# Kernel tuning notes

Hardware: AMD Instinct MI355X
Metric: run time of the kernel (lower is better)

The kernel has to match this reference:

```python
import jax, jax.numpy as jnp
import numpy as np

B, F, T, Z, Y, X = 1, 8, 5, 16, 96, 96
N_RAYS = 32768   # n_rays_scan
K = 128          # n_points_ray
NEAR_PLANE = 0.01
C = F * Z        # conv channels after folding Z into channel dim


def setup_inputs() -> dict:
    key = jax.random.key(0)
    ks = jax.random.split(key, 6)
    vol = jax.random.normal(ks[0], (B, F, T, Z, Y, X), jnp.float32)
    # ray origins inside the normalized unit-cube scene
    rays_o = jax.random.uniform(ks[1], (T, N_RAYS, 3), jnp.float32, 0.1, 0.9)
    rd = jax.random.normal(ks[2], (T, N_RAYS, 3), jnp.float32)
    rays_d = rd / jnp.linalg.norm(rd, axis=-1, keepdims=True)
    conv_w = jax.random.normal(ks[3], (C, C, 3, 3, 3), jnp.float32) * (1.0 / np.sqrt(C * 27))
    conv_b = jnp.zeros((C,), jnp.float32)
    dens_w = jax.random.normal(ks[4], (F, 1), jnp.float32) * (1.0 / np.sqrt(F))
    dens_b = jnp.zeros((1,), jnp.float32)
    return dict(curr_feat_volume=vol, ray_start=rays_o, ray_direction=rays_d,
                conv_w=conv_w, conv_b=conv_b, dens_w=dens_w, dens_b=dens_b)


def _trilinear(vol, pts):
    """vol: [F,Z,Y,X]; pts: [...,3] with (x,y,z) in [0,1]. Returns [..., F]."""
    Fc, Zs, Ys, Xs = vol.shape
    gx = jnp.clip(pts[..., 0], 0.0, 1.0) * (Xs - 1)
    gy = jnp.clip(pts[..., 1], 0.0, 1.0) * (Ys - 1)
    gz = jnp.clip(pts[..., 2], 0.0, 1.0) * (Zs - 1)
    x0 = jnp.floor(gx).astype(jnp.int32); x1 = jnp.minimum(x0 + 1, Xs - 1)
    y0 = jnp.floor(gy).astype(jnp.int32); y1 = jnp.minimum(y0 + 1, Ys - 1)
    z0 = jnp.floor(gz).astype(jnp.int32); z1 = jnp.minimum(z0 + 1, Zs - 1)
    fx = gx - x0; fy = gy - y0; fz = gz - z0
    out = 0.0
    for zi, wz in ((z0, 1 - fz), (z1, fz)):
        for yi, wy in ((y0, 1 - fy), (y1, fy)):
            for xi, wx in ((x0, 1 - fx), (x1, fx)):
                out = out + vol[:, zi, yi, xi] * (wz * wy * wx)[None]
    return jnp.moveaxis(out, 0, -1)


def _render_t(vol_t, o, d, dens_w, dens_b):
    """One timestep: vol_t [F,Z,Y,X], o/d [N,3] -> depth [N,1]."""
    # SceneCollider: AABB [0,1]^3 with near_plane clamp
    t1 = (0.0 - o) / d
    t2 = (1.0 - o) / d
    near = jnp.max(jnp.minimum(t1, t2), axis=-1, keepdims=True)
    far = jnp.min(jnp.maximum(t1, t2), axis=-1, keepdims=True)
    near = jnp.maximum(near, NEAR_PLANE)
    far = jnp.maximum(far, near + 1e-6)
    # UniformSampler (deterministic bins)
    bins = jnp.linspace(0.0, 1.0, K + 1, dtype=jnp.float32)
    ts = near + bins[None, :] * (far - near)          # [N,K+1]
    starts = ts[:, :-1, None]                          # [N,K,1]
    ends = ts[:, 1:, None]
    mids = 0.5 * (starts + ends)
    pts = o[:, None, :] + d[:, None, :] * mids         # [N,K,3]
    # DensityField: trilinear feature gather + linear + softplus
    feats = _trilinear(vol_t, pts)                     # [N,K,F]
    density = jax.nn.softplus(feats @ dens_w + dens_b) # [N,K,1]
    # weights / transmittance (alpha compositing)
    deltas = ends - starts
    dd = density * deltas
    trans = jnp.exp(-jnp.concatenate([jnp.zeros_like(dd[:, :1]),
                                      jnp.cumsum(dd[:, :-1], axis=1)], axis=1))
    alpha = 1.0 - jnp.exp(-dd)
    weights = alpha * trans                            # [N,K,1]
    # DepthRenderer
    eps = 1e-10
    depth = jnp.sum(weights * starts, axis=-2) / (jnp.sum(weights, axis=-2) + eps)
    depth = jnp.clip(depth, starts.min(), starts.max())
    return depth                                       # [N,1]


def reference(curr_feat_volume, ray_start, ray_direction, conv_w, conv_b, dens_w, dens_b):
    # fold Z into channels and run dense Conv3d over (T,Y,X)
    x = jnp.transpose(curr_feat_volume, (0, 1, 3, 2, 4, 5)).reshape(B, F * Z, T, Y, X)
    y = jax.lax.conv_general_dilated(
        x, conv_w, window_strides=(1, 1, 1), padding='SAME',
        dimension_numbers=('NCDHW', 'OIDHW', 'NCDHW'))
    y = y + conv_b[None, :, None, None, None]
    future = jnp.transpose(y.reshape(B, F, Z, T, Y, X), (0, 3, 1, 2, 4, 5))  # [B,T,F,Z,Y,X]
    vols = future[0]                                   # [T,F,Z,Y,X]
    depth = jax.vmap(lambda v, o, d: _render_t(v, o, d, dens_w, dens_b))(
        vols, ray_start, ray_direction)                # [T,N,1]
    return depth
```

## Files before the change

### kernel.cpp

```cpp
#include <hip/hip_runtime.h>
#include <hip/hip_fp16.h>
#include <cstdint>
#include <cstddef>

#define T_DIM 5
#define F_DIM 8
#define Z_DIM 16
#define Y_DIM 96
#define X_DIM 96
#define NRAYS 32768
#define K_SAMP 128


struct __align__(16) Cell { __half2 h0, h1, h2, h3; };

typedef __attribute__((ext_vector_type(4))) float     f32x4;
typedef __attribute__((ext_vector_type(8))) _Float16  f16x8;

__device__ __forceinline__ float fexp2(float x) { return __builtin_amdgcn_exp2f(x); }
__device__ __forceinline__ float flog2(float x) { return __builtin_amdgcn_logf(x); }

__global__ __launch_bounds__(256) void setup_kernel(
        const float* __restrict__ xin, __half* __restrict__ inp,
        const float* __restrict__ w, const float* __restrict__ cb,
        const float* __restrict__ dw, __half* __restrict__ wB, float* __restrict__ bR,
        const float* __restrict__ ro, const float* __restrict__ rd,
        float* __restrict__ nearA, float* __restrict__ farA) {
    int b = blockIdx.x;
    if (b < 480) {
        __shared__ __half lds[96 * 136];
        int t = b / 96, y = b - (b / 96) * 96;
        for (int i = threadIdx.x; i < 12288; i += 256) {
            int row = i / 96;
            int x   = i - row * 96;
            int f = row >> 4, z = row & 15;
            float v = xin[(((size_t)(f * 5 + t) * 16 + z) * 96 + y) * 96 + x];
            lds[x * 136 + row] = __float2half(v);
        }
        __syncthreads();
        __half* ob = inp + ((size_t)(t * 96 + y) * 96) * 128;
        for (int c = threadIdx.x; c < 1536; c += 256) {
            int x = c >> 4, sub = c & 15;
            uint4 v = *(const uint4*)(lds + x * 136 + sub * 8);
            *(uint4*)(ob + (size_t)x * 128 + sub * 8) = v;
        }
    } else if (b < 696) {
        int i = (b - 480) * 256 + threadIdx.x;
        if (i < 16) {
            float s = 0.f;
            #pragma unroll
            for (int f = 0; f < 8; ++f) s += cb[f * 16 + i] * dw[f];
            bR[i] = s;
        }
        int cs  = i & 31;
        int zo  = (i >> 5) & 15;
        int pt  = i >> 9;
        int p   = pt / 27;
        int tap = pt - p * 27;
        int ci  = p * 32 + cs;
        float s = 0.f;
        #pragma unroll
        for (int f = 0; f < 8; ++f)
            s += w[(size_t)((f * 16 + zo) * 128 + ci) * 27 + tap] * dw[f];
        wB[i] = __float2half(s);
    } else {
        int gid = (b - 696) * 256 + threadIdx.x;
        const float* o = ro + (size_t)gid * 3;
        const float* d = rd + (size_t)gid * 3;
        float ox = o[0], oy = o[1], oz = o[2];
        float dx = d[0], dy = d[1], dz = d[2];
        float t1x = (0.f - ox) / dx, t2x = (1.f - ox) / dx;
        float t1y = (0.f - oy) / dy, t2y = (1.f - oy) / dy;
        float t1z = (0.f - oz) / dz, t2z = (1.f - oz) / dz;
        float nr = fmaxf(fmaxf(fminf(t1x, t2x), fminf(t1y, t2y)), fminf(t1z, t2z));
        float fr = fminf(fminf(fmaxf(t1x, t2x), fmaxf(t1y, t2y)), fmaxf(t1z, t2z));
        nr = fmaxf(nr, 0.01f);
        fr = fmaxf(fr, nr + 1e-6f);
        nearA[gid] = nr;
        farA[gid]  = fr;
    }
}

__global__ __launch_bounds__(128) void conv_mfma_kernel(
        const __half* __restrict__ inp, const __half* __restrict__ wB,
        const float* __restrict__ bR, float* __restrict__ fld) {
    int bid = blockIdx.x;
    int wg  = (bid & 7) * 90 + (bid >> 3);
    int xs  = wg % 3;
    int rem = wg / 3;
    int yp  = rem % 48;
    int t   = rem / 48;
    int xseg = xs * 32, y0 = yp * 2;

    __shared__ __half lds[2][12 * 34 * 32];
    const int w    = threadIdx.x >> 6;
    const int lane = threadIdx.x & 63;
    const int l15  = lane & 15;
    const int ksub = lane >> 4;

    const int xl0 = threadIdx.x >> 2, sub0 = threadIdx.x & 3;
    const int xg0 = xseg + xl0 - 1;
    const bool xok0 = (unsigned)xg0 < 96u;
    const int glo0 = xg0 * 128 + sub0 * 8;
    const int lof0 = xl0 * 32 + ((sub0 ^ ((xl0 >> 1) & 3)) << 3);
    const int q    = threadIdx.x / 12;
    const int rowh = threadIdx.x - q * 12;
    const int xl1  = 32 + (q >> 2), sub1 = q & 3;
    const int xg1  = xseg + xl1 - 1;
    const bool hwr = (q < 8);
    const bool hld = hwr && ((unsigned)xg1 < 96u);
    const int glo1 = xg1 * 128 + sub1 * 8;
    const int lof1 = xl1 * 32 + ((sub1 ^ ((xl1 >> 1) & 3)) << 3);

    int offA[3];
    #pragma unroll
    for (int kx = 0; kx < 3; ++kx) {
        int X = l15 + kx;
        offA[kx] = X * 32 + ((ksub ^ ((X >> 1) & 3)) << 3);
    }

    uint4 vm[12];
    uint4 vh;
    f32x4 acc0 = {0.f, 0.f, 0.f, 0.f};
    f32x4 acc1 = {0.f, 0.f, 0.f, 0.f};

    #pragma unroll
    for (int r = 0; r < 12; ++r) {
        int tt = t + (r >> 2) - 1;
        int yy = y0 + (r & 3) - 1;
        bool rok = ((unsigned)tt < 5u) & ((unsigned)yy < 96u);
        int rbase = (tt * 96 + yy) * 12288;
        uint4 v = {0u, 0u, 0u, 0u};
        if (rok & xok0) v = *(const uint4*)(inp + rbase + glo0);
        vm[r] = v;
    }
    {
        int tt = t + (rowh >> 2) - 1;
        int yy = y0 + (rowh & 3) - 1;
        bool rok = ((unsigned)tt < 5u) & ((unsigned)yy < 96u);
        int rbase = (tt * 96 + yy) * 12288;
        uint4 v = {0u, 0u, 0u, 0u};
        if (rok & hld) v = *(const uint4*)(inp + rbase + glo1);
        vh = v;
    }

    #pragma unroll
    for (int p = 0; p < 4; ++p) {
        __half* L = &lds[p & 1][0];
        #pragma unroll
        for (int r = 0; r < 12; ++r)
            *(uint4*)(L + r * 1088 + lof0) = vm[r];
        if (hwr)
            *(uint4*)(L + rowh * 1088 + lof1) = vh;
        __syncthreads();

        if (p < 3) {
            #pragma unroll
            for (int r = 0; r < 12; ++r) {
                int tt = t + (r >> 2) - 1;
                int yy = y0 + (r & 3) - 1;
                bool rok = ((unsigned)tt < 5u) & ((unsigned)yy < 96u);
                int rbase = (tt * 96 + yy) * 12288 + ((p + 1) << 5);
                uint4 v = {0u, 0u, 0u, 0u};
                if (rok & xok0) v = *(const uint4*)(inp + rbase + glo0);
                vm[r] = v;
            }
            {
                int tt = t + (rowh >> 2) - 1;
                int yy = y0 + (rowh & 3) - 1;
                bool rok = ((unsigned)tt < 5u) & ((unsigned)yy < 96u);
                int rbase = (tt * 96 + yy) * 12288 + ((p + 1) << 5);
                uint4 v = {0u, 0u, 0u, 0u};
                if (rok & hld) v = *(const uint4*)(inp + rbase + glo1);
                vh = v;
            }
        }

        const __half* wp_base = wB + (size_t)p * 13824 + l15 * 32 + ksub * 8;
        #pragma unroll
        for (int kt = 0; kt < 3; ++kt) {
            #pragma unroll
            for (int ky = 0; ky < 3; ++ky) {
                const __half* lrow = L + (kt * 4 + w + ky) * 1088;
                #pragma unroll
                for (int kx = 0; kx < 3; ++kx) {
                    int tap = (kt * 3 + ky) * 3 + kx;
                    f16x8 aw = *(const f16x8*)(wp_base + tap * 512);
                    f16x8 b0 = *(const f16x8*)(lrow + offA[kx]);
                    acc0 = __builtin_amdgcn_mfma_f32_16x16x32_f16(aw, b0, acc0, 0, 0, 0);
                    f16x8 b1 = *(const f16x8*)(lrow + offA[kx] + 512);
                    acc1 = __builtin_amdgcn_mfma_f32_16x16x32_f16(aw, b1, acc1, 0, 0, 0);
                }
            }
        }
    }

    int yw = y0 + w;
    #pragma unroll
    for (int r = 0; r < 4; ++r) {
        int zo = ksub * 4 + r;
        float bz = bR[zo];
        size_t o = (((size_t)t * 16 + zo) * 96 + yw) * 96 + xseg + l15;
        fld[o]      = acc0[r] + bz;
        fld[o + 16] = acc1[r] + bz;
    }
}

__global__ __launch_bounds__(256) void pack_kernel(
        const float* __restrict__ fld, Cell* __restrict__ cellp) {
    int i = blockIdx.x * 256 + threadIdx.x;
    if (i >= 737280) return;
    int x = i % 96;
    int r = i / 96;
    int y = r % 96;
    int r2 = r / 96;
    int z = r2 % 16;
    int t = r2 / 16;
    const float* ft = fld + (size_t)t * 147456;
    int xp = min(x + 1, 95);
    int yr0 = y * 96, yr1 = min(y + 1, 95) * 96;
    int zr0 = z * 9216, zr1 = min(z + 1, 15) * 9216;
    float c000 = ft[zr0 + yr0 + x], c001 = ft[zr0 + yr0 + xp];
    float c010 = ft[zr0 + yr1 + x], c011 = ft[zr0 + yr1 + xp];
    float c100 = ft[zr1 + yr0 + x], c101 = ft[zr1 + yr0 + xp];
    float c110 = ft[zr1 + yr1 + x], c111 = ft[zr1 + yr1 + xp];
    Cell cl;
    cl.h0 = __floats2half2_rn(c000, c001 - c000);
    cl.h1 = __floats2half2_rn(c010, c011 - c010);
    cl.h2 = __floats2half2_rn(c100, c101 - c100);
    cl.h3 = __floats2half2_rn(c110, c111 - c110);
    cellp[i] = cl;
}

__global__ __launch_bounds__(256) void render_kernel(
        const float* __restrict__ ro, const float* __restrict__ rd,
        const Cell* __restrict__ cellp,
        const float* __restrict__ nearA, const float* __restrict__ farA,
        const float* __restrict__ dens_b, float* __restrict__ out) {
    int b = blockIdx.x;
    int b7 = b & 7, bhi = b >> 3;
    int t, seg;
    if (b7 < 5) { t = b7; seg = bhi; }
    else { int j = (b7 - 5) * 640 + bhi; t = j / 384; seg = 640 + j % 384; }
    int c = threadIdx.x & 7;
    int ray = t * NRAYS + seg * 32 + (threadIdx.x >> 3);

    const float* o = ro + (size_t)ray * 3;
    const float* d = rd + (size_t)ray * 3;
    float ox = o[0], oy = o[1], oz = o[2];
    float dx = d[0], dy = d[1], dz = d[2];
    float nr = nearA[ray], fr = farA[ray];
    const Cell* vt = cellp + (size_t)t * 147456;
    const float L2E = 1.4426950408889634f;
    float db2 = dens_b[0] * L2E;

    float span = fr - nr;
    float step = span * 0.0078125f;
    float s  = fmaf((float)(c * 16), step, nr);
    float mid = s + 0.5f * step;
    float pxg = fmaf(dx, mid, ox) * 95.f;
    float pyg = fmaf(dy, mid, oy) * 95.f;
    float pzg = fmaf(dz, mid, oz) * 15.f;
    float ddxg = dx * step * 95.f, ddyg = dy * step * 95.f, ddzg = dz * step * 15.f;

    float num = 0.f, den = 0.f, A2 = 0.f;
    float trans = 1.f;
    int pidx = -1;
    Cell cl;
    for (int kk = 0; kk < 16; ++kk) {
        int x0 = min(max((int)pxg, 0), 94);
        int y0 = min(max((int)pyg, 0), 94);
        int z0 = min(max((int)pzg, 0), 14);
        float fx = pxg - (float)x0, fy = pyg - (float)y0, fz = pzg - (float)z0;

        int idx = z0 * 9216 + y0 * 96 + x0;
        if (idx != pidx) {
            pidx = idx;
            cl = vt[idx];
        }

        float v00 = fmaf(fx, __half2float(__high2half(cl.h0)), __half2float(__low2half(cl.h0)));
        float v01 = fmaf(fx, __half2float(__high2half(cl.h1)), __half2float(__low2half(cl.h1)));
        float v10 = fmaf(fx, __half2float(__high2half(cl.h2)), __half2float(__low2half(cl.h2)));
        float v11 = fmaf(fx, __half2float(__high2half(cl.h3)), __half2float(__low2half(cl.h3)));
        float v0  = fmaf(fy, v01 - v00, v00);
        float v1  = fmaf(fy, v11 - v10, v10);
        float pre2 = fmaf(fmaf(fz, v1 - v0, v0), L2E, db2);

        float u = fexp2(-fabsf(pre2));
        float dens2 = fmaxf(pre2, 0.f) + flog2(1.f + u);
        float dd2 = dens2 * step;
        float ex = fexp2(-dd2);
        float wgt = (1.f - ex) * trans;
        num = fmaf(wgt, s, num);
        den += wgt;
        trans *= ex;
        A2 += dd2;
        s += step; pxg += ddxg; pyg += ddyg; pzg += ddzg;
    }
    int lane = threadIdx.x & 63;
    int qb = lane & ~7;
    float P = 0.f;
    #pragma unroll
    for (int j = 0; j < 7; ++j) {
        float Aj = __shfl(A2, qb + j, 64);
        P += (c > j) ? Aj : 0.f;
    }
    float sc = fexp2(-P);
    float numc = num * sc;
    float denc = den * sc;
    numc += __shfl_xor(numc, 1, 64);
    numc += __shfl_xor(numc, 2, 64);
    numc += __shfl_xor(numc, 4, 64);
    denc += __shfl_xor(denc, 1, 64);
    denc += __shfl_xor(denc, 2, 64);
    denc += __shfl_xor(denc, 4, 64);
    if (c == 0) {
        float depth = numc / (denc + 1e-10f);
        float slast = fmaf(0.9921875f, span, nr);
        depth = fminf(fmaxf(depth, nr), slast);
        out[ray] = depth;
    }
}

extern "C" void kernel_launch(void* const* d_in, const int* in_sizes, int n_in,
                              void* d_out, int out_size, void* d_ws, size_t ws_size,
                              hipStream_t stream) {
    const float* vol = (const float*)d_in[0];
    const float* ro  = (const float*)d_in[1];
    const float* rd  = (const float*)d_in[2];
    const float* cw  = (const float*)d_in[3];
    const float* cb  = (const float*)d_in[4];
    const float* dw  = (const float*)d_in[5];
    const float* dbp = (const float*)d_in[6];
    float* out = (float*)d_out;

    float* ws      = (float*)d_ws;
    float* fld     = ws;
    __half* inp    = (__half*)(ws + 737280);
    Cell*  cellp   = (Cell*)(ws + 737280);
    __half* wB     = (__half*)(ws + 737280 + 2949120);
    float* bR      = ws + 737280 + 2949120 + 27648;
    float* nearA   = bR + 32;
    float* farA    = nearA + 163840;

    hipLaunchKernelGGL(setup_kernel, dim3(1336), dim3(256), 0, stream,
                       vol, inp, cw, cb, dw, wB, bR, ro, rd, nearA, farA);
    hipLaunchKernelGGL(conv_mfma_kernel, dim3(720), dim3(128), 0, stream,
                       inp, wB, bR, fld);
    hipLaunchKernelGGL(pack_kernel, dim3(2880), dim3(256), 0, stream, fld, cellp);
    hipLaunchKernelGGL(render_kernel, dim3(5120), dim3(256), 0, stream,
                       ro, rd, cellp, nearA, farA, dbp, out);
}
```

Measured before the change: 161.4 us.

## Drop LDS staging in conv; read input directly from global with finer tiles

```diff
diff --git a/kernel.cpp b/kernel.cpp
--- a/kernel.cpp
+++ b/kernel.cpp
@@ -81,128 +81,77 @@
     }
 }
 
-__global__ __launch_bounds__(128) void conv_mfma_kernel(
+__global__ __launch_bounds__(128, 4) void conv_mfma_kernel(
         const __half* __restrict__ inp, const __half* __restrict__ wB,
         const float* __restrict__ bR, float* __restrict__ fld) {
     int bid = blockIdx.x;
-    int wg  = (bid & 7) * 90 + (bid >> 3);
+    int wg  = (bid & 7) * 180 + (bid >> 3);
     int xs  = wg % 3;
     int rem = wg / 3;
-    int yp  = rem % 48;
-    int t   = rem / 48;
-    int xseg = xs * 32, y0 = yp * 2;
-
-    __shared__ __half lds[2][12 * 34 * 32];
-    const int w    = threadIdx.x >> 6;
+    int y   = rem % 96;
+    int t   = rem / 96;
+
+    const int xt   = threadIdx.x >> 6;
     const int lane = threadIdx.x & 63;
     const int l15  = lane & 15;
     const int ksub = lane >> 4;
-
-    const int xl0 = threadIdx.x >> 2, sub0 = threadIdx.x & 3;
-    const int xg0 = xseg + xl0 - 1;
-    const bool xok0 = (unsigned)xg0 < 96u;
-    const int glo0 = xg0 * 128 + sub0 * 8;
-    const int lof0 = xl0 * 32 + ((sub0 ^ ((xl0 >> 1) & 3)) << 3);
-    const int q    = threadIdx.x / 12;
-    const int rowh = threadIdx.x - q * 12;
-    const int xl1  = 32 + (q >> 2), sub1 = q & 3;
-    const int xg1  = xseg + xl1 - 1;
-    const bool hwr = (q < 8);
-    const bool hld = hwr && ((unsigned)xg1 < 96u);
-    const int glo1 = xg1 * 128 + sub1 * 8;
-    const int lof1 = xl1 * 32 + ((sub1 ^ ((xl1 >> 1) & 3)) << 3);
-
-    int offA[3];
-    #pragma unroll
-    for (int kx = 0; kx < 3; ++kx) {
-        int X = l15 + kx;
-        offA[kx] = X * 32 + ((ksub ^ ((X >> 1) & 3)) << 3);
-    }
-
-    uint4 vm[12];
-    uint4 vh;
-    f32x4 acc0 = {0.f, 0.f, 0.f, 0.f};
-    f32x4 acc1 = {0.f, 0.f, 0.f, 0.f};
-
-    #pragma unroll
-    for (int r = 0; r < 12; ++r) {
-        int tt = t + (r >> 2) - 1;
-        int yy = y0 + (r & 3) - 1;
-        bool rok = ((unsigned)tt < 5u) & ((unsigned)yy < 96u);
-        int rbase = (tt * 96 + yy) * 12288;
-        uint4 v = {0u, 0u, 0u, 0u};
-        if (rok & xok0) v = *(const uint4*)(inp + rbase + glo0);
-        vm[r] = v;
-    }
-    {
-        int tt = t + (rowh >> 2) - 1;
-        int yy = y0 + (rowh & 3) - 1;
-        bool rok = ((unsigned)tt < 5u) & ((unsigned)yy < 96u);
-        int rbase = (tt * 96 + yy) * 12288;
-        uint4 v = {0u, 0u, 0u, 0u};
-        if (rok & hld) v = *(const uint4*)(inp + rbase + glo1);
-        vh = v;
-    }
+    const int xb   = xs * 32 + xt * 16;
+
+    const bool ok0 = (xb + l15 - 1) >= 0;
+    const bool ok2 = (xb + l15 + 1) < 96;
+    const int xh0 = max(xb + l15 - 1, 0) << 7;
+    const int xh1 = (xb + l15) << 7;
+    const int xh2 = min(xb + l15 + 1, 95) << 7;
+
+    f32x4 accA = {0.f, 0.f, 0.f, 0.f};
+    f32x4 accB = {0.f, 0.f, 0.f, 0.f};
+    const int ko = ksub * 8;
 
     #pragma unroll
     for (int p = 0; p < 4; ++p) {
-        __half* L = &lds[p & 1][0];
-        #pragma unroll
-        for (int r = 0; r < 12; ++r)
-            *(uint4*)(L + r * 1088 + lof0) = vm[r];
-        if (hwr)
-            *(uint4*)(L + rowh * 1088 + lof1) = vh;
-        __syncthreads();
-
-        if (p < 3) {
-            #pragma unroll
-            for (int r = 0; r < 12; ++r) {
-                int tt = t + (r >> 2) - 1;
-                int yy = y0 + (r & 3) - 1;
-                bool rok = ((unsigned)tt < 5u) & ((unsigned)yy < 96u);
-                int rbase = (tt * 96 + yy) * 12288 + ((p + 1) << 5);
-                uint4 v = {0u, 0u, 0u, 0u};
-                if (rok & xok0) v = *(const uint4*)(inp + rbase + glo0);
-                vm[r] = v;
-            }
-            {
-                int tt = t + (rowh >> 2) - 1;
-                int yy = y0 + (rowh & 3) - 1;
-                bool rok = ((unsigned)tt < 5u) & ((unsigned)yy < 96u);
-                int rbase = (tt * 96 + yy) * 12288 + ((p + 1) << 5);
-                uint4 v = {0u, 0u, 0u, 0u};
-                if (rok & hld) v = *(const uint4*)(inp + rbase + glo1);
-                vh = v;
-            }
-        }
-
-        const __half* wp_base = wB + (size_t)p * 13824 + l15 * 32 + ksub * 8;
+        const __half* wpb = wB + p * 13824 + l15 * 32 + ko;
         #pragma unroll
         for (int kt = 0; kt < 3; ++kt) {
+            int tt = t + kt - 1;
+            if ((unsigned)tt >= 5u) continue;
             #pragma unroll
             for (int ky = 0; ky < 3; ++ky) {
-                const __half* lrow = L + (kt * 4 + w + ky) * 1088;
-                #pragma unroll
-                for (int kx = 0; kx < 3; ++kx) {
-                    int tap = (kt * 3 + ky) * 3 + kx;
-                    f16x8 aw = *(const f16x8*)(wp_base + tap * 512);
-                    f16x8 b0 = *(const f16x8*)(lrow + offA[kx]);
-                    acc0 = __builtin_amdgcn_mfma_f32_16x16x32_f16(aw, b0, acc0, 0, 0, 0);
-                    f16x8 b1 = *(const f16x8*)(lrow + offA[kx] + 512);
-                    acc1 = __builtin_amdgcn_mfma_f32_16x16x32_f16(aw, b1, acc1, 0, 0, 0);
+                int yy = y + ky - 1;
+                if ((unsigned)yy >= 96u) continue;
+                const __half* rb = inp + (size_t)(tt * 96 + yy) * 12288 + (p << 5) + ko;
+                const int tapb = (kt * 3 + ky) * 3;
+                {
+                    f16x8 aw = *(const f16x8*)(wpb + tapb * 512);
+                    uint4 bv = *(const uint4*)(rb + xh0);
+                    if (!ok0) bv = make_uint4(0u, 0u, 0u, 0u);
+                    f16x8 bb = *(f16x8*)&bv;
+                    if (tapb & 1) accB = __builtin_amdgcn_mfma_f32_16x16x32_f16(aw, bb, accB, 0, 0, 0);
+                    else          accA = __builtin_amdgcn_mfma_f32_16x16x32_f16(aw, bb, accA, 0, 0, 0);
+                }
+                {
+                    f16x8 aw = *(const f16x8*)(wpb + (tapb + 1) * 512);
+                    f16x8 bb = *(const f16x8*)(rb + xh1);
+                    if ((tapb + 1) & 1) accB = __builtin_amdgcn_mfma_f32_16x16x32_f16(aw, bb, accB, 0, 0, 0);
+                    else                accA = __builtin_amdgcn_mfma_f32_16x16x32_f16(aw, bb, accA, 0, 0, 0);
+                }
+                {
+                    f16x8 aw = *(const f16x8*)(wpb + (tapb + 2) * 512);
+                    uint4 bv = *(const uint4*)(rb + xh2);
+                    if (!ok2) bv = make_uint4(0u, 0u, 0u, 0u);
+                    f16x8 bb = *(f16x8*)&bv;
+                    if ((tapb + 2) & 1) accB = __builtin_amdgcn_mfma_f32_16x16x32_f16(aw, bb, accB, 0, 0, 0);
+                    else                accA = __builtin_amdgcn_mfma_f32_16x16x32_f16(aw, bb, accA, 0, 0, 0);
                 }
             }
         }
     }
 
-    int yw = y0 + w;
     #pragma unroll
     for (int r = 0; r < 4; ++r) {
         int zo = ksub * 4 + r;
         float bz = bR[zo];
-        size_t o = (((size_t)t * 16 + zo) * 96 + yw) * 96 + xseg + l15;
-        fld[o]      = acc0[r] + bz;
-        fld[o + 16] = acc1[r] + bz;
+        size_t o = (((size_t)t * 16 + zo) * 96 + y) * 96 + xb + l15;
+        fld[o] = accA[r] + accB[r] + bz;
     }
 }
 
@@ -346,7 +295,7 @@
 
     hipLaunchKernelGGL(setup_kernel, dim3(1336), dim3(256), 0, stream,
                        vol, inp, cw, cb, dw, wB, bR, ro, rd, nearA, farA);
-    hipLaunchKernelGGL(conv_mfma_kernel, dim3(720), dim3(128), 0, stream,
+    hipLaunchKernelGGL(conv_mfma_kernel, dim3(1440), dim3(128), 0, stream,
                        inp, wB, bR, fld);
     hipLaunchKernelGGL(pack_kernel, dim3(2880), dim3(256), 0, stream, fld, cellp);
     hipLaunchKernelGGL(render_kernel, dim3(5120), dim3(256), 0, stream,
```

Result: slower. 195.5 us (+21.1%).

## Split conv reduction over input-channel chunks across blocks and add combine kernel

Applied to the files above, without the earlier changes.

```diff
diff --git a/kernel.cpp b/kernel.cpp
--- a/kernel.cpp
+++ b/kernel.cpp
@@ -83,16 +83,18 @@
 
 __global__ __launch_bounds__(128) void conv_mfma_kernel(
         const __half* __restrict__ inp, const __half* __restrict__ wB,
-        const float* __restrict__ bR, float* __restrict__ fld) {
+        float* __restrict__ part) {
     int bid = blockIdx.x;
-    int wg  = (bid & 7) * 90 + (bid >> 3);
-    int xs  = wg % 3;
-    int rem = wg / 3;
+    int wg  = (bid & 7) * 360 + (bid >> 3);
+    int p   = wg & 3;
+    int wq  = wg >> 2;
+    int xs  = wq % 3;
+    int rem = wq / 3;
     int yp  = rem % 48;
     int t   = rem / 48;
     int xseg = xs * 32, y0 = yp * 2;
 
-    __shared__ __half lds[2][12 * 34 * 32];
+    __shared__ __half lds[12 * 34 * 32];
     const int w    = threadIdx.x >> 6;
     const int lane = threadIdx.x & 63;
     const int l15  = lane & 15;
@@ -101,7 +103,7 @@
     const int xl0 = threadIdx.x >> 2, sub0 = threadIdx.x & 3;
     const int xg0 = xseg + xl0 - 1;
     const bool xok0 = (unsigned)xg0 < 96u;
-    const int glo0 = xg0 * 128 + sub0 * 8;
+    const int glo0 = xg0 * 128 + sub0 * 8 + (p << 5);
     const int lof0 = xl0 * 32 + ((sub0 ^ ((xl0 >> 1) & 3)) << 3);
     const int q    = threadIdx.x / 12;
     const int rowh = threadIdx.x - q * 12;
@@ -109,7 +111,7 @@
     const int xg1  = xseg + xl1 - 1;
     const bool hwr = (q < 8);
     const bool hld = hwr && ((unsigned)xg1 < 96u);
-    const int glo1 = xg1 * 128 + sub1 * 8;
+    const int glo1 = xg1 * 128 + sub1 * 8 + (p << 5);
     const int lof1 = xl1 * 32 + ((sub1 ^ ((xl1 >> 1) & 3)) << 3);
 
     int offA[3];
@@ -120,10 +122,6 @@
     }
 
     uint4 vm[12];
-    uint4 vh;
-    f32x4 acc0 = {0.f, 0.f, 0.f, 0.f};
-    f32x4 acc1 = {0.f, 0.f, 0.f, 0.f};
-
     #pragma unroll
     for (int r = 0; r < 12; ++r) {
         int tt = t + (r >> 2) - 1;
@@ -134,76 +132,67 @@
         if (rok & xok0) v = *(const uint4*)(inp + rbase + glo0);
         vm[r] = v;
     }
+    uint4 vh = {0u, 0u, 0u, 0u};
     {
         int tt = t + (rowh >> 2) - 1;
         int yy = y0 + (rowh & 3) - 1;
         bool rok = ((unsigned)tt < 5u) & ((unsigned)yy < 96u);
         int rbase = (tt * 96 + yy) * 12288;
-        uint4 v = {0u, 0u, 0u, 0u};
-        if (rok & hld) v = *(const uint4*)(inp + rbase + glo1);
-        vh = v;
-    }
-
-    #pragma unroll
-    for (int p = 0; p < 4; ++p) {
-        __half* L = &lds[p & 1][0];
+        if (rok & hld) vh = *(const uint4*)(inp + rbase + glo1);
+    }
+    #pragma unroll
+    for (int r = 0; r < 12; ++r)
+        *(uint4*)(lds + r * 1088 + lof0) = vm[r];
+    if (hwr)
+        *(uint4*)(lds + rowh * 1088 + lof1) = vh;
+    __syncthreads();
+
+    f32x4 acc0 = {0.f, 0.f, 0.f, 0.f};
+    f32x4 acc1 = {0.f, 0.f, 0.f, 0.f};
+    const __half* wp_base = wB + (size_t)p * 13824 + l15 * 32 + ksub * 8;
+    #pragma unroll
+    for (int kt = 0; kt < 3; ++kt) {
         #pragma unroll
-        for (int r = 0; r < 12; ++r)
-            *(uint4*)(L + r * 1088 + lof0) = vm[r];
-        if (hwr)
-            *(uint4*)(L + rowh * 1088 + lof1) = vh;
-        __syncthreads();
-
-        if (p < 3) {
+        for (int ky = 0; ky < 3; ++ky) {
+            const __half* lrow = lds + (kt * 4 + w + ky) * 1088;
             #pragma unroll
-            for (int r = 0; r < 12; ++r) {
-                int tt = t + (r >> 2) - 1;
-                int yy = y0 + (r & 3) - 1;
-                bool rok = ((unsigned)tt < 5u) & ((unsigned)yy < 96u);
-                int rbase = (tt * 96 + yy) * 12288 + ((p + 1) << 5);
-                uint4 v = {0u, 0u, 0u, 0u};
-                if (rok & xok0) v = *(const uint4*)(inp + rbase + glo0);
-                vm[r] = v;
+            for (int kx = 0; kx < 3; ++kx) {
+                int tap = (kt * 3 + ky) * 3 + kx;
+                f16x8 aw = *(const f16x8*)(wp_base + tap * 512);
+                f16x8 b0 = *(const f16x8*)(lrow + offA[kx]);
+                acc0 = __builtin_amdgcn_mfma_f32_16x16x32_f16(aw, b0, acc0, 0, 0, 0);
+                f16x8 b1 = *(const f16x8*)(lrow + offA[kx] + 512);
+                acc1 = __builtin_amdgcn_mfma_f32_16x16x32_f16(aw, b1, acc1, 0, 0, 0);
             }
-            {
-                int tt = t + (rowh >> 2) - 1;
-                int yy = y0 + (rowh & 3) - 1;
-                bool rok = ((unsigned)tt < 5u) & ((unsigned)yy < 96u);
-                int rbase = (tt * 96 + yy) * 12288 + ((p + 1) << 5);
-                uint4 v = {0u, 0u, 0u, 0u};
-                if (rok & hld) v = *(const uint4*)(inp + rbase + glo1);
-                vh = v;
-            }
-        }
-
-        const __half* wp_base = wB + (size_t)p * 13824 + l15 * 32 + ksub * 8;
-        #pragma unroll
-        for (int kt = 0; kt < 3; ++kt) {
-            #pragma unroll
-            for (int ky = 0; ky < 3; ++ky) {
-                const __half* lrow = L + (kt * 4 + w + ky) * 1088;
-                #pragma unroll
-                for (int kx = 0; kx < 3; ++kx) {
-                    int tap = (kt * 3 + ky) * 3 + kx;
-                    f16x8 aw = *(const f16x8*)(wp_base + tap * 512);
-                    f16x8 b0 = *(const f16x8*)(lrow + offA[kx]);
-                    acc0 = __builtin_amdgcn_mfma_f32_16x16x32_f16(aw, b0, acc0, 0, 0, 0);
-                    f16x8 b1 = *(const f16x8*)(lrow + offA[kx] + 512);
-                    acc1 = __builtin_amdgcn_mfma_f32_16x16x32_f16(aw, b1, acc1, 0, 0, 0);
-                }
-            }
         }
     }
 
     int yw = y0 + w;
+    float* po = part + (size_t)p * 737280;
     #pragma unroll
     for (int r = 0; r < 4; ++r) {
         int zo = ksub * 4 + r;
-        float bz = bR[zo];
         size_t o = (((size_t)t * 16 + zo) * 96 + yw) * 96 + xseg + l15;
-        fld[o]      = acc0[r] + bz;
-        fld[o + 16] = acc1[r] + bz;
-    }
+        po[o]      = acc0[r];
+        po[o + 16] = acc1[r];
+    }
+}
+
+__global__ __launch_bounds__(256) void combine_kernel(
+        const float* __restrict__ part, const float* __restrict__ bR,
+        float* __restrict__ fld) {
+    int i = blockIdx.x * 256 + threadIdx.x;
+    if (i >= 184320) return;
+    int z = (i / 2304) & 15;
+    float b = bR[z];
+    float4 r = make_float4(b, b, b, b);
+    const float4* pp = (const float4*)part;
+    #pragma unroll
+    for (int s = 0; s < 4; ++s) {
+        float4 a = pp[(size_t)s * 184320 + i];
+        r.x += a.x; r.y += a.y; r.z += a.z; r.w += a.w;
+    }
+    ((float4*)fld)[i] = r;
 }
 
 __global__ __launch_bounds__(256) void pack_kernel(
@@ -343,11 +332,14 @@
     float* bR      = ws + 737280 + 2949120 + 27648;
     float* nearA   = bR + 32;
     float* farA    = nearA + 163840;
+    float* part    = farA + 163840;
 
     hipLaunchKernelGGL(setup_kernel, dim3(1336), dim3(256), 0, stream,
                        vol, inp, cw, cb, dw, wB, bR, ro, rd, nearA, farA);
-    hipLaunchKernelGGL(conv_mfma_kernel, dim3(720), dim3(128), 0, stream,
-                       inp, wB, bR, fld);
+    hipLaunchKernelGGL(conv_mfma_kernel, dim3(2880), dim3(128), 0, stream,
+                       inp, wB, part);
+    hipLaunchKernelGGL(combine_kernel, dim3(720), dim3(256), 0, stream,
+                       part, bR, fld);
     hipLaunchKernelGGL(pack_kernel, dim3(2880), dim3(256), 0, stream, fld, cellp);
     hipLaunchKernelGGL(render_kernel, dim3(5120), dim3(256), 0, stream,
                        ro, rd, cellp, nearA, farA, dbp, out);
```

Result: no change. 161.0 us (-0.2%).
